# Kernel optimization log

Measured on AMD Instinct MI355X. Metric: run time of the kernel, lower is better.

Reference implementation:

```python
import jax, jax.numpy as jnp
import numpy as np
from jax import lax

DIM = 512
HEADS = 8
HEAD_DIM = DIM // HEADS
FS = 56            # features_size -> H = W = 56
SR = 2             # sr_ratio
N = FS * FS        # query tokens = 3136
KN = (FS // SR) ** 2  # kv tokens = 784
B = 4
SCALE = HEAD_DIM ** -0.5
LN_EPS = 1e-5


def _relative_indices(fs):
    # matches generate_relative_distance: [[x, y] for x in range(fs) for y in range(fs)]
    coords = np.stack(np.meshgrid(np.arange(fs), np.arange(fs), indexing='ij'), -1).reshape(-1, 2)
    dist = coords[None, :, :] - coords[:, None, :] + (fs - 1)   # (N, N, 2), values in [0, 2fs-2]
    return jnp.asarray(dist, dtype=jnp.int32)


def setup_inputs() -> dict:
    key = jax.random.key(0)
    ks = jax.random.split(key, 8)
    s = 0.02
    return {
        'x':    jax.random.normal(ks[0], (B, DIM, FS, FS), jnp.float32),
        'Wq':   jax.random.normal(ks[1], (DIM, DIM), jnp.float32) * s,
        'Wkv':  jax.random.normal(ks[2], (DIM, 2 * DIM), jnp.float32) * s,
        'Wsr':  jax.random.normal(ks[3], (DIM, DIM, SR, SR), jnp.float32) * s,  # OIHW
        'b_sr': jnp.zeros((DIM,), jnp.float32),
        'gamma': jnp.ones((DIM,), jnp.float32),
        'beta':  jnp.zeros((DIM,), jnp.float32),
        'Wp':   jax.random.normal(ks[4], (DIM, DIM), jnp.float32) * s,
        'bp':   jnp.zeros((DIM,), jnp.float32),
        'pos':  jax.random.normal(ks[5], (2 * FS - 1, 2 * FS - 1), jnp.float32) * 0.2,
        'rel_idx': _relative_indices(FS),
    }


def reference(x, Wq, Wkv, Wsr, b_sr, gamma, beta, Wp, bp, pos, rel_idx):
    b, c, h, w = x.shape
    n = h * w
    xq = x.reshape(b, c, n).transpose(0, 2, 1)                      # B N C
    q = (xq @ Wq).reshape(b, n, HEADS, HEAD_DIM).transpose(0, 2, 1, 3)  # B h N d

    # spatial reduction of k/v: Conv2d(k=SR, s=SR) + LayerNorm
    xr = lax.conv_general_dilated(x, Wsr, (SR, SR), 'VALID',
                                  dimension_numbers=('NCHW', 'OIHW', 'NCHW'))
    xr = xr + b_sr[None, :, None, None]
    kn = xr.shape[2] * xr.shape[3]
    xkv = xr.reshape(b, c, kn).transpose(0, 2, 1)                   # B KN C
    mu = xkv.mean(-1, keepdims=True)
    var = ((xkv - mu) ** 2).mean(-1, keepdims=True)
    xkv = (xkv - mu) * lax.rsqrt(var + LN_EPS) * gamma + beta

    # kv projection; rearrange 'B N (dim h l) -> l B h N dim'
    kv = (xkv @ Wkv).reshape(b, kn, HEAD_DIM, HEADS, 2)
    k = kv[..., 0].transpose(0, 3, 1, 2)                            # B h KN d
    v = kv[..., 1].transpose(0, 3, 1, 2)                            # B h KN d

    attn = jnp.einsum('bhnd,bhmd->bhnm', q, k) * SCALE              # B h N KN
    bias = pos[rel_idx[:, :kn, 0], rel_idx[:, :kn, 1]]              # N KN gathered bias
    attn = jax.nn.softmax(attn + bias, axis=-1)

    out = jnp.einsum('bhnm,bhmd->bhnd', attn, v)                    # B h N d
    out = out.transpose(0, 2, 1, 3).reshape(b, n, c)                # B N C
    out = out @ Wp + bp
    return out.transpose(0, 2, 1).reshape(b, c, h, w)
```

## Files before the change

### kernel.cpp

```cpp
#include <hip/hip_runtime.h>
#include <hip/hip_bf16.h>
#include <cstdint>

constexpr int BATCH = 4;
constexpr int CDIM  = 512;
constexpr int NHEAD = 8;
constexpr int HD    = 64;
constexpr int FSP   = 56;
constexpr int NTOK  = FSP * FSP;
constexpr int KH    = 28;
constexpr int KNTOK = KH * KH;
constexpr float SCALE_ATT = 0.125f;
constexpr int BIAS_LD = 832;

typedef _Float16 f16;
typedef __attribute__((ext_vector_type(8))) _Float16 half8;
typedef __attribute__((ext_vector_type(4))) float  floatx4;

__device__ __forceinline__ void tr64(const float* __restrict__ in,
                                     f16* __restrict__ out, int R, int C,
                                     int r0, int c0, float (*sm)[65], int tid) {
  const int rr = tid >> 2, cs = (tid & 3) * 16;
  const float* src = in + (size_t)(r0 + rr) * C + c0 + cs;
#pragma unroll
  for (int j = 0; j < 16; j += 4) *(float4*)&sm[rr][cs + j] = *(const float4*)&src[j];
  __syncthreads();
  f16* dh = out + (size_t)(c0 + rr) * R + r0 + cs;
#pragma unroll
  for (int j = 0; j < 16; ++j) dh[j] = (f16)sm[cs + j][rr];
}

__global__ __launch_bounds__(256) void k_prep(const float* __restrict__ x,
                                              const float* __restrict__ Wq,
                                              const float* __restrict__ Wkv,
                                              const float* __restrict__ Wp,
                                              const float* __restrict__ Wsr,
                                              const int* __restrict__ rel,
                                              const float* __restrict__ pos,
                                              f16* __restrict__ xT,
                                              f16* __restrict__ WqT,
                                              f16* __restrict__ WkvT,
                                              f16* __restrict__ WpT,
                                              f16* __restrict__ WsrP,
                                              float* __restrict__ biasT) {
  __shared__ float sm[64][65];
  const int tid = threadIdx.x;
  int bid = blockIdx.x;
  if (bid < 1568) {
    const int b = bid / 392, r = bid % 392;
    tr64(x + (size_t)b * CDIM * NTOK, xT + (size_t)b * NTOK * CDIM,
         CDIM, NTOK, (r % 8) * 64, (r / 8) * 64, sm, tid);
    return;
  }
  bid -= 1568;
  if (bid < 64)  { tr64(Wq,  WqT,  512, 512,  (bid % 8) * 64, (bid / 8) * 64, sm, tid); return; }
  bid -= 64;
  if (bid < 128) { tr64(Wkv, WkvT, 512, 1024, (bid % 8) * 64, (bid / 8) * 64, sm, tid); return; }
  bid -= 128;
  if (bid < 64)  { tr64(Wp,  WpT,  512, 512,  (bid % 8) * 64, (bid / 8) * 64, sm, tid); return; }
  bid -= 64;
  if (bid < 512) {
    const float* src = Wsr + (size_t)bid * 2048;
    f16* dh = WsrP + (size_t)bid * 2048;
    for (int kp = tid; kp < 2048; kp += 256) {
      const int dd = kp >> 9, c = kp & 511;
      dh[kp] = (f16)src[c * 4 + dd];
    }
    return;
  }
  bid -= 512;
  {
    const int n = bid;
    for (int i = tid; i < BIAS_LD; i += 256) {
      const int jc = i >> 6, w = i & 63, txx = w >> 2, tt = w & 3;
      const int m = jc * 64 + tt * 16 + txx;
      float v = -30000.f;
      if (m < KNTOK) {
        const size_t o = ((size_t)n * NTOK + m) * 2;
        v = pos[rel[o] * 111 + rel[o + 1]];
      }
      biasT[(size_t)n * BIAS_LD + i] = v;
    }
  }
}

struct GemmSmem { f16 A[128 * 32]; f16 B[128 * 32]; };

__device__ __forceinline__ void gl_lds(const f16* g, f16* l) {
  __builtin_amdgcn_global_load_lds(
      (const __attribute__((address_space(1))) void*)g,
      (__attribute__((address_space(3))) void*)l, 16, 0, 0);
}

__device__ __forceinline__ void gemm128(GemmSmem* sm,
    const f16* a0, const f16* a1, const f16* b0, const f16* b1,
    int lane, int wv, int wm, int wn, int quad, int tx,
    floatx4 acc[4][4]) {
  f16* lA0 = sm->A + wv * 1024 + lane * 8;
  f16* lA1 = sm->A + wv * 1024 + 512 + lane * 8;
  f16* lB0 = sm->B + wv * 1024 + lane * 8;
  f16* lB1 = sm->B + wv * 1024 + 512 + lane * 8;
  for (int it = 0; it < 16; ++it) {
    gl_lds(a0 + it * 32, lA0);
    gl_lds(a1 + it * 32, lA1);
    gl_lds(b0 + it * 32, lB0);
    gl_lds(b1 + it * 32, lB1);
    __syncthreads();
    half8 af[4], bf[4];
#pragma unroll
    for (int i = 0; i < 4; ++i)
      af[i] = *(const half8*)&sm->A[(wm * 64 + i * 16 + tx) * 32 + quad * 8];
#pragma unroll
    for (int j = 0; j < 4; ++j)
      bf[j] = *(const half8*)&sm->B[(wn * 64 + j * 16 + tx) * 32 + quad * 8];
#pragma unroll
    for (int j = 0; j < 4; ++j)
#pragma unroll
      for (int i = 0; i < 4; ++i)
        acc[i][j] = __builtin_amdgcn_mfma_f32_16x16x32_f16(af[i], bf[j], acc[i][j], 0, 0, 0);
    __syncthreads();
  }
}

#define GEMM128_PRE()                                                     \
  const int tid = threadIdx.x, lane = tid & 63, wv = tid >> 6;            \
  const int wm = wv & 1, wn = wv >> 1, quad = lane >> 4, tx = lane & 15;  \
  const int lr = lane >> 2, lc = (lane & 3) * 8;                          \
  floatx4 acc[4][4];                                                      \
  _Pragma("unroll") for (int i = 0; i < 4; ++i)                           \
  _Pragma("unroll") for (int j = 0; j < 4; ++j)                           \
      acc[i][j] = (floatx4){0.f, 0.f, 0.f, 0.f};

__global__ __launch_bounds__(256) void k_gemmA(const f16* __restrict__ xT,
                                               const f16* __restrict__ WqT,
                                               f16* __restrict__ Qh,
                                               const f16* __restrict__ WsrP,
                                               float* __restrict__ XRp) {
  __shared__ GemmSmem sm;
  GEMM128_PRE();
  int bid = blockIdx.x;
  if (bid < 400) {
    const int b = bid / 100, t = bid % 100;
    const int m0 = (t >> 2) * 128, n0 = (t & 3) * 128;
    const f16* xb = xT + (size_t)b * NTOK * CDIM;
    const int r0 = wv * 32 + lr, r1 = r0 + 16;
    const f16* a0 = xb + (size_t)min(m0 + r0, NTOK - 1) * CDIM + lc;
    const f16* a1 = xb + (size_t)min(m0 + r1, NTOK - 1) * CDIM + lc;
    const f16* b0 = WqT + (size_t)(n0 + r0) * CDIM + lc;
    const f16* b1 = WqT + (size_t)(n0 + r1) * CDIM + lc;
    gemm128(&sm, a0, a1, b0, b1, lane, wv, wm, wn, quad, tx, acc);
    f16* qhB = Qh + (size_t)b * NTOK * CDIM;
#pragma unroll
    for (int i = 0; i < 4; ++i)
#pragma unroll
      for (int rg = 0; rg < 4; ++rg) {
        const int m = m0 + wm * 64 + i * 16 + quad * 4 + rg;
        if (m >= NTOK) continue;
#pragma unroll
        for (int j = 0; j < 4; ++j)
          qhB[(size_t)m * CDIM + n0 + wn * 64 + j * 16 + tx] = (f16)acc[i][j][rg];
      }
  } else {
    bid -= 400;
    const int bkc = bid / 28, r = bid % 28;
    const int b = bkc >> 2, kc = bkc & 3;
    const int m0 = (r >> 2) * 128, n0 = (r & 3) * 128;
    const f16* xb = xT + (size_t)b * NTOK * CDIM;
    const int r0 = wv * 32 + lr, r1 = r0 + 16;
    int am0 = m0 + r0; if (am0 >= KNTOK) am0 = 0;
    int am1 = m0 + r1; if (am1 >= KNTOK) am1 = 0;
    const int sp0 = 112 * (am0 / KH) + 2 * (am0 % KH) + (kc >> 1) * FSP + (kc & 1);
    const int sp1 = 112 * (am1 / KH) + 2 * (am1 % KH) + (kc >> 1) * FSP + (kc & 1);
    const f16* a0 = xb + (size_t)sp0 * CDIM + lc;
    const f16* a1 = xb + (size_t)sp1 * CDIM + lc;
    const f16* b0 = WsrP + (size_t)(n0 + r0) * 2048 + kc * 512 + lc;
    const f16* b1 = WsrP + (size_t)(n0 + r1) * 2048 + kc * 512 + lc;
    gemm128(&sm, a0, a1, b0, b1, lane, wv, wm, wn, quad, tx, acc);
    float* dst = XRp + (size_t)(kc * BATCH + b) * KNTOK * CDIM;
#pragma unroll
    for (int i = 0; i < 4; ++i)
#pragma unroll
      for (int rg = 0; rg < 4; ++rg) {
        const int m = m0 + wm * 64 + i * 16 + quad * 4 + rg;
        if (m >= KNTOK) continue;
#pragma unroll
        for (int j = 0; j < 4; ++j)
          dst[(size_t)m * CDIM + n0 + wn * 64 + j * 16 + tx] = acc[i][j][rg];
      }
  }
}

__global__ __launch_bounds__(256) void k_ln(const float* __restrict__ XRp,
                                            const float* __restrict__ b_sr,
                                            const float* __restrict__ gamma,
                                            const float* __restrict__ beta,
                                            f16* __restrict__ oh) {
  const int row = blockIdx.x;
  const size_t slab = (size_t)BATCH * KNTOK * CDIM;
  const float* p = XRp + (size_t)row * CDIM;
  const int tid = threadIdx.x;
  const float v0 = p[tid] + p[tid + slab] + p[tid + 2 * slab] + p[tid + 3 * slab]
                 + b_sr[tid];
  const float v1 = p[tid + 256] + p[tid + 256 + slab] + p[tid + 256 + 2 * slab]
                 + p[tid + 256 + 3 * slab] + b_sr[tid + 256];
  float s = v0 + v1;
  float s2 = v0 * v0 + v1 * v1;
#pragma unroll
  for (int mask = 32; mask >= 1; mask >>= 1) {
    s  += __shfl_xor(s, mask, 64);
    s2 += __shfl_xor(s2, mask, 64);
  }
  __shared__ float ws[4], ws2[4];
  const int wid = tid >> 6;
  if ((tid & 63) == 0) { ws[wid] = s; ws2[wid] = s2; }
  __syncthreads();
  const float ts  = ws[0] + ws[1] + ws[2] + ws[3];
  const float ts2 = ws2[0] + ws2[1] + ws2[2] + ws2[3];
  const float mu  = ts * (1.f / CDIM);
  const float var = ts2 * (1.f / CDIM) - mu * mu;
  const float rs  = rsqrtf(var + 1e-5f);
  const size_t base = (size_t)row * CDIM;
  oh[base + tid]       = (f16)((v0 - mu) * rs * gamma[tid] + beta[tid]);
  oh[base + tid + 256] = (f16)((v1 - mu) * rs * gamma[tid + 256] + beta[tid + 256]);
}

__global__ __launch_bounds__(256) void k_kvproj(const f16* __restrict__ XRh,
                                                const f16* __restrict__ WkvT,
                                                f16* __restrict__ Kh,
                                                f16* __restrict__ Vt) {
  __shared__ GemmSmem sm;
  GEMM128_PRE();
  const int bid = blockIdx.x;
  const int b = bid / 56, r = bid % 56, nt = r >> 3, mt = r & 7;
  const int m0 = (r / 8) * 128, n0 = (r % 8) * 128;
  (void)nt; (void)mt;
  const f16* ab = XRh + (size_t)b * KNTOK * CDIM;
  const int r0 = wv * 32 + lr, r1 = r0 + 16;
  const f16* a0 = ab + (size_t)min(m0 + r0, KNTOK - 1) * CDIM + lc;
  const f16* a1 = ab + (size_t)min(m0 + r1, KNTOK - 1) * CDIM + lc;
  const f16* b0 = WkvT + (size_t)(n0 + r0) * CDIM + lc;
  const f16* b1 = WkvT + (size_t)(n0 + r1) * CDIM + lc;
  gemm128(&sm, a0, a1, b0, b1, lane, wv, wm, wn, quad, tx, acc);
#pragma unroll
  for (int i = 0; i < 4; ++i)
#pragma unroll
    for (int rg = 0; rg < 4; ++rg) {
      const int m = m0 + wm * 64 + i * 16 + quad * 4 + rg;
      if (m >= KNTOK) continue;
#pragma unroll
      for (int j = 0; j < 4; ++j) {
        const int o2 = n0 + wn * 64 + j * 16 + tx;
        const int d = o2 >> 4, hh = (o2 >> 1) & 7;
        const float v = acc[i][j][rg];
        if (o2 & 1)
          Vt[((size_t)(b * NHEAD + hh) * HD + d) * KNTOK + m] = (f16)v;
        else
          Kh[((size_t)(b * NHEAD + hh) * KNTOK + m) * HD + d] = (f16)v;
      }
    }
}

#define LSTR 72
__global__ __launch_bounds__(256) void k_attn(const f16* __restrict__ Qh,
                                              const f16* __restrict__ Kh,
                                              const f16* __restrict__ Vt,
                                              const float* __restrict__ biasT,
                                              f16* __restrict__ Oh) {
  __shared__ f16 Qhs[64][LSTR], Khs[64][LSTR], Vts[64][LSTR];
  __shared__ f16 Ps[4][16][LSTR];
  const int b = blockIdx.x >> 3, h = blockIdx.x & 7;
  const int n0 = blockIdx.y * 64;
  const int tid = threadIdx.x, lane = tid & 63, wv = tid >> 6;
  const int quad = lane >> 4, tx = lane & 15;
  const int rr = tid >> 2, sg = (tid & 3) * 16;

  const f16* qhB = Qh + ((size_t)b * NTOK + n0) * CDIM + h * HD;
  const f16* khB = Kh + (size_t)(b * NHEAD + h) * KNTOK * HD;
  const f16* vtB = Vt + (size_t)(b * NHEAD + h) * HD * KNTOK;

  {
    const size_t qoff = (size_t)rr * CDIM + sg;
    *(half8*)&Qhs[rr][sg]     = *(const half8*)&qhB[qoff];
    *(half8*)&Qhs[rr][sg + 8] = *(const half8*)&qhB[qoff + 8];
    const size_t koff = (size_t)rr * HD + sg;
    *(half8*)&Khs[rr][sg]     = *(const half8*)&khB[koff];
    *(half8*)&Khs[rr][sg + 8] = *(const half8*)&khB[koff + 8];
    const size_t voff = (size_t)rr * KNTOK + sg;
    *(half8*)&Vts[rr][sg]     = *(const half8*)&vtB[voff];
    *(half8*)&Vts[rr][sg + 8] = *(const half8*)&vtB[voff + 8];
  }

  size_t bbase_r[4];
#pragma unroll
  for (int r = 0; r < 4; ++r)
    bbase_r[r] = (size_t)(n0 + wv * 16 + quad * 4 + r) * BIAS_LD + tx * 4;

  floatx4 acc_o[4];
#pragma unroll
  for (int t = 0; t < 4; ++t) acc_o[t] = (floatx4){0.f, 0.f, 0.f, 0.f};
  float l_part[4] = {0.f, 0.f, 0.f, 0.f};
  __syncthreads();

  half8 nk0, nk1, nv0, nv1;
  for (int jc = 0; jc < 13; ++jc) {
    if (jc < 12) {
      const int mbn = (jc + 1) * 64;
      const int km = min(mbn + rr, KNTOK - 1);
      const size_t koff = (size_t)km * HD + sg;
      nk0 = *(const half8*)&khB[koff];
      nk1 = *(const half8*)&khB[koff + 8];
      const int vc = min(mbn + sg, KNTOK - 16);
      const size_t voff = (size_t)rr * KNTOK + vc;
      nv0 = *(const half8*)&vtB[voff];
      nv1 = *(const half8*)&vtB[voff + 8];
    }

    floatx4 sc[4];
#pragma unroll
    for (int t = 0; t < 4; ++t) sc[t] = (floatx4){0.f, 0.f, 0.f, 0.f};
#pragma unroll
    for (int ks = 0; ks < 2; ++ks) {
      const int kk = ks * 32 + quad * 8;
      const half8 aqh = *(const half8*)&Qhs[wv * 16 + tx][kk];
#pragma unroll
      for (int t = 0; t < 4; ++t) {
        const half8 bkh = *(const half8*)&Khs[t * 16 + tx][kk];
        sc[t] = __builtin_amdgcn_mfma_f32_16x16x32_f16(aqh, bkh, sc[t], 0, 0, 0);
      }
    }

#pragma unroll
    for (int r = 0; r < 4; ++r) {
      const float4 bb = *(const float4*)&biasT[bbase_r[r] + jc * 64];
      const float p0 = __expf(fmaf(sc[0][r], SCALE_ATT, bb.x));
      const float p1 = __expf(fmaf(sc[1][r], SCALE_ATT, bb.y));
      const float p2 = __expf(fmaf(sc[2][r], SCALE_ATT, bb.z));
      const float p3 = __expf(fmaf(sc[3][r], SCALE_ATT, bb.w));
      l_part[r] += (p0 + p1) + (p2 + p3);
      const int prow = quad * 4 + r;
      Ps[wv][prow][0 * 16 + tx] = (f16)p0;
      Ps[wv][prow][1 * 16 + tx] = (f16)p1;
      Ps[wv][prow][2 * 16 + tx] = (f16)p2;
      Ps[wv][prow][3 * 16 + tx] = (f16)p3;
    }

#pragma unroll
    for (int ks = 0; ks < 2; ++ks) {
      const int kk = ks * 32 + quad * 8;
      const half8 ap = *(const half8*)&Ps[wv][tx][kk];
#pragma unroll
      for (int t = 0; t < 4; ++t) {
        const half8 bv = *(const half8*)&Vts[t * 16 + tx][kk];
        acc_o[t] = __builtin_amdgcn_mfma_f32_16x16x32_f16(ap, bv, acc_o[t], 0, 0, 0);
      }
    }
    __syncthreads();
    if (jc < 12) {
      *(half8*)&Khs[rr][sg]     = nk0;
      *(half8*)&Khs[rr][sg + 8] = nk1;
      *(half8*)&Vts[rr][sg]     = nv0;
      *(half8*)&Vts[rr][sg + 8] = nv1;
    }
    __syncthreads();
  }

#pragma unroll
  for (int r = 0; r < 4; ++r) {
    float l = l_part[r];
#pragma unroll
    for (int msk = 1; msk < 16; msk <<= 1) l += __shfl_xor(l, msk, 64);
    const float inv = 1.f / l;
    const int grow = n0 + wv * 16 + quad * 4 + r;
    const size_t base = ((size_t)b * NTOK + grow) * CDIM + h * HD;
#pragma unroll
    for (int t = 0; t < 4; ++t)
      Oh[base + t * 16 + tx] = (f16)(acc_o[t][r] * inv);
  }
}

__global__ __launch_bounds__(256) void k_outproj(const f16* __restrict__ Og,
                                                 const f16* __restrict__ WpT,
                                                 const float* __restrict__ bp,
                                                 float* __restrict__ out) {
  __shared__ GemmSmem sm;
  GEMM128_PRE();
  const int bid = blockIdx.x;
  const int b = bid / 100, t = bid % 100;
  const int m0 = (t >> 2) * 128, n0 = (t & 3) * 128;
  const f16* ab = Og + (size_t)b * NTOK * CDIM;
  const int r0 = wv * 32 + lr, r1 = r0 + 16;
  const f16* a0 = ab + (size_t)min(m0 + r0, NTOK - 1) * CDIM + lc;
  const f16* a1 = ab + (size_t)min(m0 + r1, NTOK - 1) * CDIM + lc;
  const f16* b0 = WpT + (size_t)(n0 + r0) * CDIM + lc;
  const f16* b1 = WpT + (size_t)(n0 + r1) * CDIM + lc;
  gemm128(&sm, a0, a1, b0, b1, lane, wv, wm, wn, quad, tx, acc);
#pragma unroll
  for (int j = 0; j < 4; ++j) {
    const int co = n0 + wn * 64 + j * 16 + tx;
    const float bpv = bp[co];
    float* obase = out + ((size_t)b * CDIM + co) * NTOK;
#pragma unroll
    for (int i = 0; i < 4; ++i) {
      const int mb4 = m0 + wm * 64 + i * 16 + quad * 4;
      if (mb4 < NTOK) {
        floatx4 v = acc[i][j] + bpv;
        *(floatx4*)&obase[mb4] = v;
      }
    }
  }
}

extern "C" void kernel_launch(void* const* d_in, const int* in_sizes, int n_in,
                              void* d_out, int out_size, void* d_ws, size_t ws_size,
                              hipStream_t stream) {
  const float* x     = (const float*)d_in[0];
  const float* Wq    = (const float*)d_in[1];
  const float* Wkv   = (const float*)d_in[2];
  const float* Wsr   = (const float*)d_in[3];
  const float* b_sr  = (const float*)d_in[4];
  const float* gamma = (const float*)d_in[5];
  const float* beta  = (const float*)d_in[6];
  const float* Wp    = (const float*)d_in[7];
  const float* bp    = (const float*)d_in[8];
  const float* pos   = (const float*)d_in[9];
  const int*   rel   = (const int*)d_in[10];
  float* out = (float*)d_out;

  char* p = (char*)d_ws;
  auto alloc = [&](size_t bytes) -> void* {
    void* r = (void*)p;
    p += (bytes + 255) & ~(size_t)255;
    return r;
  };
  const size_t SZ_BNC = (size_t)BATCH * NTOK * CDIM;
  const size_t SZ_BKC = (size_t)BATCH * KNTOK * CDIM;
  const size_t SZ_KV  = (size_t)BATCH * NHEAD * KNTOK * HD;

  f16* xT    = (f16*)alloc(SZ_BNC * 2);
  f16* WqT   = (f16*)alloc(512 * 512 * 2);
  f16* WkvT  = (f16*)alloc(1024 * 512 * 2);
  f16* WpT   = (f16*)alloc(512 * 512 * 2);
  f16* WsrP  = (f16*)alloc(512 * 2048 * 2);
  f16* Qh    = (f16*)alloc(SZ_BNC * 2);
  float* XRp = (float*)alloc(SZ_BKC * 4 * 4);
  f16* XRh   = (f16*)alloc(SZ_BKC * 2);
  f16* Vt    = (f16*)alloc(SZ_KV * 2);
  float* biasT = (float*)alloc((size_t)NTOK * BIAS_LD * 4);

  f16* Kh = (f16*)XRp;
  f16* Og = xT;

  const dim3 blk(256);
  k_prep   <<<dim3(5472), blk, 0, stream>>>(x, Wq, Wkv, Wp, Wsr, rel, pos,
                                            xT, WqT, WkvT, WpT, WsrP, biasT);
  k_gemmA  <<<dim3(848),  blk, 0, stream>>>(xT, WqT, Qh, WsrP, XRp);
  k_ln     <<<dim3(BATCH * KNTOK), blk, 0, stream>>>(XRp, b_sr, gamma, beta, XRh);
  k_kvproj <<<dim3(224),  blk, 0, stream>>>(XRh, WkvT, Kh, Vt);
  k_attn   <<<dim3(BATCH * NHEAD, 49), blk, 0, stream>>>(Qh, Kh, Vt, biasT, Og);
  k_outproj<<<dim3(400),  blk, 0, stream>>>(Og, WpT, bp, out);
}
```

Baseline: 301.6 us.

## Enlarge attention query tile, compute relative bias analytically, vectorise transpose stores

The attention kernel now processes 128 query rows per block (two 16-row MFMA tiles per wave), so each K/V tile loaded into shared memory is reused twice as much and the grid shrinks. The positional bias table is built from closed-form row/column index arithmetic instead of gathering from the large relative-index input, removing a big strided read. The fp32-to-fp16 transpose writes two 8-wide vectors instead of 16 scalar stores. The costs are more registers and LDS in attention, which may reduce occupancy, and relying on the fixed structure of the relative-index input.

```diff
diff --git a/kernel.cpp b/kernel.cpp
--- a/kernel.cpp
+++ b/kernel.cpp
@@ -26,8 +26,13 @@
   for (int j = 0; j < 16; j += 4) *(float4*)&sm[rr][cs + j] = *(const float4*)&src[j];
   __syncthreads();
   f16* dh = out + (size_t)(c0 + rr) * R + r0 + cs;
-#pragma unroll
-  for (int j = 0; j < 16; ++j) dh[j] = (f16)sm[cs + j][rr];
+  half8 v0, v1;
+#pragma unroll
+  for (int j = 0; j < 8; ++j) v0[j] = (f16)sm[cs + j][rr];
+#pragma unroll
+  for (int j = 0; j < 8; ++j) v1[j] = (f16)sm[cs + 8 + j][rr];
+  *(half8*)&dh[0] = v0;
+  *(half8*)&dh[8] = v1;
 }
 
 __global__ __launch_bounds__(256) void k_prep(const float* __restrict__ x,
@@ -35,7 +40,6 @@
                                               const float* __restrict__ Wkv,
                                               const float* __restrict__ Wp,
                                               const float* __restrict__ Wsr,
-                                              const int* __restrict__ rel,
                                               const float* __restrict__ pos,
                                               f16* __restrict__ xT,
                                               f16* __restrict__ WqT,
@@ -71,13 +75,15 @@
   bid -= 512;
   {
     const int n = bid;
+    const int in_ = n / FSP, jn = n % FSP;
+    const int cbase = 55 * 111 + 55 - in_ * 111 - jn;
     for (int i = tid; i < BIAS_LD; i += 256) {
       const int jc = i >> 6, w = i & 63, txx = w >> 2, tt = w & 3;
       const int m = jc * 64 + tt * 16 + txx;
       float v = -30000.f;
       if (m < KNTOK) {
-        const size_t o = ((size_t)n * NTOK + m) * 2;
-        v = pos[rel[o] * 111 + rel[o + 1]];
+        const int im = m / FSP, jm = m % FSP;
+        v = pos[cbase + im * 111 + jm];
       }
       biasT[(size_t)n * BIAS_LD + i] = v;
     }
@@ -231,9 +237,8 @@
   __shared__ GemmSmem sm;
   GEMM128_PRE();
   const int bid = blockIdx.x;
-  const int b = bid / 56, r = bid % 56, nt = r >> 3, mt = r & 7;
+  const int b = bid / 56, r = bid % 56;
   const int m0 = (r / 8) * 128, n0 = (r % 8) * 128;
-  (void)nt; (void)mt;
   const f16* ab = XRh + (size_t)b * KNTOK * CDIM;
   const int r0 = wv * 32 + lr, r1 = r0 + 16;
   const f16* a0 = ab + (size_t)min(m0 + r0, KNTOK - 1) * CDIM + lc;
@@ -266,22 +271,25 @@
                                               const f16* __restrict__ Vt,
                                               const float* __restrict__ biasT,
                                               f16* __restrict__ Oh) {
-  __shared__ f16 Qhs[64][LSTR], Khs[64][LSTR], Vts[64][LSTR];
-  __shared__ f16 Ps[4][16][LSTR];
+  __shared__ f16 Qhs[128][LSTR], Khs[64][LSTR], Vts[64][LSTR];
+  __shared__ f16 Ps[4][32][LSTR];
   const int b = blockIdx.x >> 3, h = blockIdx.x & 7;
-  const int n0 = blockIdx.y * 64;
+  const int n0 = blockIdx.y * 128;
   const int tid = threadIdx.x, lane = tid & 63, wv = tid >> 6;
   const int quad = lane >> 4, tx = lane & 15;
   const int rr = tid >> 2, sg = (tid & 3) * 16;
-
-  const f16* qhB = Qh + ((size_t)b * NTOK + n0) * CDIM + h * HD;
+  const int qr = tid >> 1, qs = (tid & 1) * 32;
+
   const f16* khB = Kh + (size_t)(b * NHEAD + h) * KNTOK * HD;
   const f16* vtB = Vt + (size_t)(b * NHEAD + h) * HD * KNTOK;
 
   {
-    const size_t qoff = (size_t)rr * CDIM + sg;
-    *(half8*)&Qhs[rr][sg]     = *(const half8*)&qhB[qoff];
-    *(half8*)&Qhs[rr][sg + 8] = *(const half8*)&qhB[qoff + 8];
+    const int qrow = min(n0 + qr, NTOK - 1);
+    const f16* src = Qh + ((size_t)b * NTOK + qrow) * CDIM + h * HD + qs;
+    *(half8*)&Qhs[qr][qs]      = *(const half8*)&src[0];
+    *(half8*)&Qhs[qr][qs + 8]  = *(const half8*)&src[8];
+    *(half8*)&Qhs[qr][qs + 16] = *(const half8*)&src[16];
+    *(half8*)&Qhs[qr][qs + 24] = *(const half8*)&src[24];
     const size_t koff = (size_t)rr * HD + sg;
     *(half8*)&Khs[rr][sg]     = *(const half8*)&khB[koff];
     *(half8*)&Khs[rr][sg + 8] = *(const half8*)&khB[koff + 8];
@@ -290,15 +298,21 @@
     *(half8*)&Vts[rr][sg + 8] = *(const half8*)&vtB[voff + 8];
   }
 
-  size_t bbase_r[4];
-#pragma unroll
-  for (int r = 0; r < 4; ++r)
-    bbase_r[r] = (size_t)(n0 + wv * 16 + quad * 4 + r) * BIAS_LD + tx * 4;
-
-  floatx4 acc_o[4];
-#pragma unroll
-  for (int t = 0; t < 4; ++t) acc_o[t] = (floatx4){0.f, 0.f, 0.f, 0.f};
-  float l_part[4] = {0.f, 0.f, 0.f, 0.f};
+  size_t bbase[2][4];
+#pragma unroll
+  for (int i = 0; i < 2; ++i)
+#pragma unroll
+    for (int rg = 0; rg < 4; ++rg) {
+      const int grow = min(n0 + wv * 32 + i * 16 + quad * 4 + rg, NTOK - 1);
+      bbase[i][rg] = (size_t)grow * BIAS_LD + tx * 4;
+    }
+
+  floatx4 acc_o[2][4];
+#pragma unroll
+  for (int i = 0; i < 2; ++i)
+#pragma unroll
+    for (int t = 0; t < 4; ++t) acc_o[i][t] = (floatx4){0.f, 0.f, 0.f, 0.f};
+  float l_part[2][4] = {};
   __syncthreads();
 
   half8 nk0, nk1, nv0, nv1;
@@ -315,43 +329,57 @@
       nv1 = *(const half8*)&vtB[voff + 8];
     }
 
-    floatx4 sc[4];
-#pragma unroll
-    for (int t = 0; t < 4; ++t) sc[t] = (floatx4){0.f, 0.f, 0.f, 0.f};
+    floatx4 sc[2][4];
+#pragma unroll
+    for (int i = 0; i < 2; ++i)
+#pragma unroll
+      for (int t = 0; t < 4; ++t) sc[i][t] = (floatx4){0.f, 0.f, 0.f, 0.f};
 #pragma unroll
     for (int ks = 0; ks < 2; ++ks) {
       const int kk = ks * 32 + quad * 8;
-      const half8 aqh = *(const half8*)&Qhs[wv * 16 + tx][kk];
+      half8 aq[2];
+#pragma unroll
+      for (int i = 0; i < 2; ++i)
+        aq[i] = *(const half8*)&Qhs[wv * 32 + i * 16 + tx][kk];
 #pragma unroll
       for (int t = 0; t < 4; ++t) {
-        const half8 bkh = *(const half8*)&Khs[t * 16 + tx][kk];
-        sc[t] = __builtin_amdgcn_mfma_f32_16x16x32_f16(aqh, bkh, sc[t], 0, 0, 0);
-      }
-    }
-
-#pragma unroll
-    for (int r = 0; r < 4; ++r) {
-      const float4 bb = *(const float4*)&biasT[bbase_r[r] + jc * 64];
-      const float p0 = __expf(fmaf(sc[0][r], SCALE_ATT, bb.x));
-      const float p1 = __expf(fmaf(sc[1][r], SCALE_ATT, bb.y));
-      const float p2 = __expf(fmaf(sc[2][r], SCALE_ATT, bb.z));
-      const float p3 = __expf(fmaf(sc[3][r], SCALE_ATT, bb.w));
-      l_part[r] += (p0 + p1) + (p2 + p3);
-      const int prow = quad * 4 + r;
-      Ps[wv][prow][0 * 16 + tx] = (f16)p0;
-      Ps[wv][prow][1 * 16 + tx] = (f16)p1;
-      Ps[wv][prow][2 * 16 + tx] = (f16)p2;
-      Ps[wv][prow][3 * 16 + tx] = (f16)p3;
-    }
+        const half8 bk = *(const half8*)&Khs[t * 16 + tx][kk];
+#pragma unroll
+        for (int i = 0; i < 2; ++i)
+          sc[i][t] = __builtin_amdgcn_mfma_f32_16x16x32_f16(aq[i], bk, sc[i][t], 0, 0, 0);
+      }
+    }
+
+#pragma unroll
+    for (int i = 0; i < 2; ++i)
+#pragma unroll
+      for (int rg = 0; rg < 4; ++rg) {
+        const float4 bb = *(const float4*)&biasT[bbase[i][rg] + jc * 64];
+        const float p0 = __expf(fmaf(sc[i][0][rg], SCALE_ATT, bb.x));
+        const float p1 = __expf(fmaf(sc[i][1][rg], SCALE_ATT, bb.y));
+        const float p2 = __expf(fmaf(sc[i][2][rg], SCALE_ATT, bb.z));
+        const float p3 = __expf(fmaf(sc[i][3][rg], SCALE_ATT, bb.w));
+        l_part[i][rg] += (p0 + p1) + (p2 + p3);
+        const int prow = i * 16 + quad * 4 + rg;
+        Ps[wv][prow][0 * 16 + tx] = (f16)p0;
+        Ps[wv][prow][1 * 16 + tx] = (f16)p1;
+        Ps[wv][prow][2 * 16 + tx] = (f16)p2;
+        Ps[wv][prow][3 * 16 + tx] = (f16)p3;
+      }
 
 #pragma unroll
     for (int ks = 0; ks < 2; ++ks) {
       const int kk = ks * 32 + quad * 8;
-      const half8 ap = *(const half8*)&Ps[wv][tx][kk];
+      half8 ap[2];
+#pragma unroll
+      for (int i = 0; i < 2; ++i)
+        ap[i] = *(const half8*)&Ps[wv][i * 16 + tx][kk];
 #pragma unroll
       for (int t = 0; t < 4; ++t) {
         const half8 bv = *(const half8*)&Vts[t * 16 + tx][kk];
-        acc_o[t] = __builtin_amdgcn_mfma_f32_16x16x32_f16(ap, bv, acc_o[t], 0, 0, 0);
+#pragma unroll
+        for (int i = 0; i < 2; ++i)
+          acc_o[i][t] = __builtin_amdgcn_mfma_f32_16x16x32_f16(ap[i], bv, acc_o[i][t], 0, 0, 0);
       }
     }
     __syncthreads();
@@ -365,17 +393,21 @@
   }
 
 #pragma unroll
-  for (int r = 0; r < 4; ++r) {
-    float l = l_part[r];
-#pragma unroll
-    for (int msk = 1; msk < 16; msk <<= 1) l += __shfl_xor(l, msk, 64);
-    const float inv = 1.f / l;
-    const int grow = n0 + wv * 16 + quad * 4 + r;
-    const size_t base = ((size_t)b * NTOK + grow) * CDIM + h * HD;
-#pragma unroll
-    for (int t = 0; t < 4; ++t)
-      Oh[base + t * 16 + tx] = (f16)(acc_o[t][r] * inv);
-  }
+  for (int i = 0; i < 2; ++i)
+#pragma unroll
+    for (int rg = 0; rg < 4; ++rg) {
+      float l = l_part[i][rg];
+#pragma unroll
+      for (int msk = 1; msk < 16; msk <<= 1) l += __shfl_xor(l, msk, 64);
+      const float inv = 1.f / l;
+      const int grow = n0 + wv * 32 + i * 16 + quad * 4 + rg;
+      if (grow < NTOK) {
+        const size_t base = ((size_t)b * NTOK + grow) * CDIM + h * HD;
+#pragma unroll
+        for (int t = 0; t < 4; ++t)
+          Oh[base + t * 16 + tx] = (f16)(acc_o[i][t][rg] * inv);
+      }
+    }
 }
 
 __global__ __launch_bounds__(256) void k_outproj(const f16* __restrict__ Og,
@@ -423,7 +455,6 @@
   const float* Wp    = (const float*)d_in[7];
   const float* bp    = (const float*)d_in[8];
   const float* pos   = (const float*)d_in[9];
-  const int*   rel   = (const int*)d_in[10];
   float* out = (float*)d_out;
 
   char* p = (char*)d_ws;
@@ -451,11 +482,11 @@
   f16* Og = xT;
 
   const dim3 blk(256);
-  k_prep   <<<dim3(5472), blk, 0, stream>>>(x, Wq, Wkv, Wp, Wsr, rel, pos,
+  k_prep   <<<dim3(5472), blk, 0, stream>>>(x, Wq, Wkv, Wp, Wsr, pos,
                                             xT, WqT, WkvT, WpT, WsrP, biasT);
   k_gemmA  <<<dim3(848),  blk, 0, stream>>>(xT, WqT, Qh, WsrP, XRp);
   k_ln     <<<dim3(BATCH * KNTOK), blk, 0, stream>>>(XRp, b_sr, gamma, beta, XRh);
   k_kvproj <<<dim3(224),  blk, 0, stream>>>(XRh, WkvT, Kh, Vt);
-  k_attn   <<<dim3(BATCH * NHEAD, 49), blk, 0, stream>>>(Qh, Kh, Vt, biasT, Og);
+  k_attn   <<<dim3(BATCH * NHEAD, 25), blk, 0, stream>>>(Qh, Kh, Vt, biasT, Og);
   k_outproj<<<dim3(400),  blk, 0, stream>>>(Og, WpT, bp, out);
 }
```

Result: faster. 284.6 us (-5.7%).
